# Optimization experiments

Hardware: AMD Instinct MI355X
Metric: run time of the kernel (lower is better)

## Reference

```python
import jax, jax.numpy as jnp
from jax import lax
import numpy as np

DEPTH = 6
DIM = 512            # embed_dim
DI = 768             # d_inner = int(1.5 * 512)
B = 64
IMG = 224
P = 16               # patch size == stride
HW = 14              # patches per side
NP = HW * HW         # 196


def _ln(x, w, b, eps=1e-5):
    m = jnp.mean(x, axis=-1, keepdims=True)
    v = jnp.var(x, axis=-1, keepdims=True)
    return (x - m) / jnp.sqrt(v + eps) * w + b


def _mamba(x, in_w, out_w, cw, cb, dw, db, A, D):
    # x: (N, L, DIM); in_w: (2*DI, DIM); out_w: (DIM, DI); cw: (DI, 3)
    xz = jnp.einsum('nlc,dc->nld', x, in_w)          # (N, L, 2*DI)
    xi, z = jnp.split(xz, 2, axis=-1)
    # depthwise conv1d, kernel=3, padding=1
    xp = jnp.pad(xi, ((0, 0), (1, 1), (0, 0)))
    xc = xp[:, :-2] * cw[:, 0] + xp[:, 1:-1] * cw[:, 1] + xp[:, 2:] * cw[:, 2] + cb
    xc = jax.nn.silu(xc)
    dt = jax.nn.softplus(jnp.einsum('nld,ed->nle', xc, dw) + db)
    Ae = jnp.exp(A * dt)                              # A < 0, dt > 0 -> stable
    y = jnp.cumsum(xc * dt * Ae, axis=1) * Ae + xc * D
    y = y * jax.nn.silu(z)
    return jnp.einsum('nld,cd->nlc', y, out_w)


def _forward(x, patch_w, patch_b, cls_token, pos_embed,
             blk_norm_w, blk_norm_b,
             mh_in_w, mh_out_w, mh_conv_w, mh_conv_b, mh_dt_w, mh_dt_b, mh_A, mh_D,
             mv_in_w, mv_out_w, mv_conv_w, mv_conv_b, mv_dt_w, mv_dt_b, mv_A, mv_D,
             fus_w, fus_b, ss_norm_w, ss_norm_b, fn_w, fn_b):
    Bsz = x.shape[0]
    # patch embed: Conv2d(3, DIM, k=16, s=16)
    feat = lax.conv_general_dilated(x, patch_w, window_strides=(P, P), padding='VALID',
                                    dimension_numbers=('NCHW', 'OIHW', 'NCHW'))
    feat = feat + patch_b[None, :, None, None]
    feat = feat.reshape(Bsz, DIM, NP).transpose(0, 2, 1)  # (B, 196, DIM)
    tok = jnp.concatenate([jnp.broadcast_to(cls_token, (Bsz, 1, DIM)), feat], axis=1)
    tok = tok + pos_embed                                  # (B, 197, DIM)
    for i in range(DEPTH):
        cls = tok[:, :1]
        pt = tok[:, 1:]
        pn = _ln(pt, blk_norm_w[i], blk_norm_b[i])
        p2 = pn.reshape(Bsz, HW, HW, DIM)
        # horizontal scan: rows as sequences
        yh = _mamba(p2.reshape(Bsz * HW, HW, DIM),
                    mh_in_w[i], mh_out_w[i], mh_conv_w[i], mh_conv_b[i],
                    mh_dt_w[i], mh_dt_b[i], mh_A[i], mh_D[i]).reshape(Bsz, HW, HW, DIM)
        # vertical scan: columns as sequences
        xv = p2.transpose(0, 2, 1, 3).reshape(Bsz * HW, HW, DIM)
        yv = _mamba(xv,
                    mv_in_w[i], mv_out_w[i], mv_conv_w[i], mv_conv_b[i],
                    mv_dt_w[i], mv_dt_b[i], mv_A[i], mv_D[i])
        yv = yv.reshape(Bsz, HW, HW, DIM).transpose(0, 2, 1, 3)
        yc = jnp.concatenate([yh, yv], axis=-1)            # (B, H, W, 2*DIM)
        yf = jnp.einsum('bhwk,ck->bhwc', yc, fus_w[i]) + fus_b[i]
        p_out = _ln(yf + p2, ss_norm_w[i], ss_norm_b[i]).reshape(Bsz, NP, DIM)
        cls_out = cls + _ln(cls, blk_norm_w[i], blk_norm_b[i])
        tok = jnp.concatenate([cls_out, p_out], axis=1)
    return _ln(tok, fn_w, fn_b)


def setup_inputs() -> dict:
    key = jax.random.key(0)
    ks = jax.random.split(key, 32)
    s = 0.02
    d = {}
    d['x'] = jax.random.normal(ks[0], (B, 3, IMG, IMG), jnp.float32)
    d['patch_w'] = jax.random.normal(ks[1], (DIM, 3, P, P), jnp.float32) * s
    d['patch_b'] = jnp.zeros((DIM,), jnp.float32)
    d['cls_token'] = jax.random.normal(ks[2], (1, 1, DIM), jnp.float32) * s
    d['pos_embed'] = jax.random.normal(ks[3], (1, NP + 1, DIM), jnp.float32) * s
    d['blk_norm_w'] = jnp.ones((DEPTH, DIM), jnp.float32)
    d['blk_norm_b'] = jnp.zeros((DEPTH, DIM), jnp.float32)
    for pfx, base in (('mh', 4), ('mv', 12)):
        d[pfx + '_in_w'] = jax.random.normal(ks[base + 0], (DEPTH, 2 * DI, DIM), jnp.float32) * s
        d[pfx + '_out_w'] = jax.random.normal(ks[base + 1], (DEPTH, DIM, DI), jnp.float32) * s
        d[pfx + '_conv_w'] = jax.random.normal(ks[base + 2], (DEPTH, DI, 3), jnp.float32) * 0.2
        d[pfx + '_conv_b'] = jnp.zeros((DEPTH, DI), jnp.float32)
        d[pfx + '_dt_w'] = jax.random.normal(ks[base + 3], (DEPTH, DI, DI), jnp.float32) * s
        d[pfx + '_dt_b'] = jnp.zeros((DEPTH, DI), jnp.float32)
        d[pfx + '_A'] = -jax.random.uniform(ks[base + 4], (DEPTH, DI), jnp.float32) * 0.1
        d[pfx + '_D'] = jnp.ones((DEPTH, DI), jnp.float32)
    d['fus_w'] = jax.random.normal(ks[20], (DEPTH, DIM, 2 * DIM), jnp.float32) * s
    d['fus_b'] = jnp.zeros((DEPTH, DIM), jnp.float32)
    d['ss_norm_w'] = jnp.ones((DEPTH, DIM), jnp.float32)
    d['ss_norm_b'] = jnp.zeros((DEPTH, DIM), jnp.float32)
    d['fn_w'] = jnp.ones((DIM,), jnp.float32)
    d['fn_b'] = jnp.zeros((DIM,), jnp.float32)
    return d


def reference(x, patch_w, patch_b, cls_token, pos_embed,
              blk_norm_w, blk_norm_b,
              mh_in_w, mh_out_w, mh_conv_w, mh_conv_b, mh_dt_w, mh_dt_b, mh_A, mh_D,
              mv_in_w, mv_out_w, mv_conv_w, mv_conv_b, mv_dt_w, mv_dt_b, mv_A, mv_D,
              fus_w, fus_b, ss_norm_w, ss_norm_b, fn_w, fn_b):
    return _forward(x, patch_w, patch_b, cls_token, pos_embed,
                    blk_norm_w, blk_norm_b,
                    mh_in_w, mh_out_w, mh_conv_w, mh_conv_b, mh_dt_w, mh_dt_b, mh_A, mh_D,
                    mv_in_w, mv_out_w, mv_conv_w, mv_conv_b, mv_dt_w, mv_dt_b, mv_A, mv_D,
                    fus_w, fus_b, ss_norm_w, ss_norm_b, fn_w, fn_b)
```

## Files before the change

kernel.cpp:

```cpp
#include <hip/hip_runtime.h>
#include <cstdint>


using u16 = unsigned short;
typedef __attribute__((ext_vector_type(8))) short   bfrag;
typedef __attribute__((ext_vector_type(4))) float   ffrag;
typedef __attribute__((ext_vector_type(8))) u16     u16x8;
typedef __attribute__((ext_vector_type(4))) u16     u16x4;

__device__ __forceinline__ float b2f(u16 u) {
  union { float f; uint32_t i; } c; c.i = ((uint32_t)u) << 16; return c.f;
}
__device__ __forceinline__ u16 f2b(float f) {
  union { float f; uint32_t i; } c; c.f = f;
  uint32_t r = c.i + 0x7FFFu + ((c.i >> 16) & 1u);
  return (u16)(r >> 16);
}

#define LOG2E 1.44269504f
#define LN2   0.69314718f
__device__ __forceinline__ float fexp(float x) {
  return __builtin_amdgcn_exp2f(x * LOG2E);
}
__device__ __forceinline__ float fsigmoid(float x) {
  return __builtin_amdgcn_rcpf(1.f + __builtin_amdgcn_exp2f(-x * LOG2E));
}
__device__ __forceinline__ float fsilu(float x) { return x * fsigmoid(x); }
__device__ __forceinline__ float fsoftplus(float x) {
  float e = __builtin_amdgcn_exp2f(-fabsf(x) * LOG2E);
  return fmaxf(x, 0.f) + LN2 * __builtin_amdgcn_logf(1.f + e);
}

__device__ __forceinline__ void gl_lds16(const u16* g, u16* l) {
  __builtin_amdgcn_global_load_lds(
      (const __attribute__((address_space(1))) void*)g,
      (__attribute__((address_space(3))) void*)l,
      16, 0, 0);
}

__global__ __launch_bounds__(256, 2)
void gemm_dual(const u16* __restrict__ A, const u16* __restrict__ W1,
               const u16* __restrict__ W2, u16* __restrict__ C,
               int K, int lda, int ldc, int nsplit, int acol2, int ccol2)
{
  __shared__ u16 As[2][128 * 64];
  __shared__ u16 Bs[2][128 * 64];

  const int total = gridDim.x * gridDim.y;
  const int flat  = blockIdx.y * gridDim.x + blockIdx.x;
  const int chunk = total >> 3;
  const int f2    = (flat & 7) * chunk + (flat >> 3);
  const int bx    = f2 % gridDim.x;
  const int by    = f2 / gridDim.x;

  const bool second = bx >= nsplit;
  const u16* W     = second ? W2 : W1;
  const int n0l    = (bx - (second ? nsplit : 0)) * 128;
  const int acol   = second ? acol2 : 0;
  const int ccol0  = n0l + (second ? ccol2 : 0);
  const int m0     = by * 128;

  const int tid  = threadIdx.x;
  const int lane = tid & 63;
  const int wv   = tid >> 6;
  const int wm   = wv >> 1;
  const int wn   = wv & 1;

  const int lr   = lane >> 3;
  const int lc   = lane & 7;
  const int kcol = (lc ^ lr) << 3;

  const size_t abase = (size_t)(m0 + wv * 32 + lr) * lda + acol + kcol;
  const size_t wbase = (size_t)(n0l + wv * 32 + lr) * K + kcol;

  const ffrag fz = {0.f, 0.f, 0.f, 0.f};
  ffrag acc[4][4];
#pragma unroll
  for (int i = 0; i < 4; ++i)
#pragma unroll
    for (int j = 0; j < 4; ++j) acc[i][j] = fz;

  const int fr = lane & 15;
  const int fq = lane >> 4;

  auto stage = [&](int kb, int buf) {
#pragma unroll
    for (int i = 0; i < 4; ++i)
      gl_lds16(A + abase + (size_t)(i * 8) * lda + kb, &As[buf][(wv * 4 + i) * 512]);
#pragma unroll
    for (int i = 0; i < 4; ++i)
      gl_lds16(W + wbase + (size_t)(i * 8) * K + kb, &Bs[buf][(wv * 4 + i) * 512]);
  };

  const int nk = K >> 6;
  stage(0, 0);
  __syncthreads();

  for (int t = 0; t < nk; ++t) {
    const int cur = t & 1;
    if (t + 1 < nk) stage((t + 1) * 64, cur ^ 1);

#pragma unroll
    for (int ks = 0; ks < 2; ++ks) {
      bfrag af[4], bfr[4];
#pragma unroll
      for (int t4 = 0; t4 < 4; ++t4) {
        int r  = wm * 64 + t4 * 16 + fr;
        int ca = ((ks * 4 + fq) ^ (r & 7)) << 3;
        af[t4]  = *(const bfrag*)&As[cur][r * 64 + ca];
        int n  = wn * 64 + t4 * 16 + fr;
        int cb = ((ks * 4 + fq) ^ (n & 7)) << 3;
        bfr[t4] = *(const bfrag*)&Bs[cur][n * 64 + cb];
      }
#pragma unroll
      for (int i = 0; i < 4; ++i)
#pragma unroll
        for (int j = 0; j < 4; ++j)
          acc[i][j] = __builtin_amdgcn_mfma_f32_16x16x32_bf16(
              af[i], bfr[j], acc[i][j], 0, 0, 0);
    }
    __syncthreads();
  }

#pragma unroll
  for (int i = 0; i < 4; ++i)
#pragma unroll
    for (int j = 0; j < 4; ++j)
#pragma unroll
      for (int rg = 0; rg < 4; ++rg) {
        int row = m0 + wm * 64 + i * 16 + fq * 4 + rg;
        int col = ccol0 + wn * 64 + j * 16 + fr;
        C[(size_t)row * ldc + col] = f2b(acc[i][j][rg]);
      }
}

__global__ __launch_bounds__(256, 2)
void gemm_wprep(const u16* __restrict__ WB, const u16* __restrict__ OT,
                u16* __restrict__ WF)
{
  __shared__ u16 As[128 * 64];
  __shared__ u16 Bs[128 * 64];

  const int z = blockIdx.z, L = z >> 1, path = z & 1;
  const u16* A = WB + (size_t)L * 4063232 + 3538944;
  const u16* W = OT + (size_t)z * 393216;
  u16* C = WF + (size_t)L * 786432;

  const int m0 = blockIdx.y * 128, n0l = blockIdx.x * 128;
  const int acol = path * 512, ccol = path * 768;

  const int tid  = threadIdx.x;
  const int lane = tid & 63;
  const int wv   = tid >> 6;
  const int wm   = wv >> 1;
  const int wn   = wv & 1;
  const int lr   = lane >> 3;
  const int lc   = lane & 7;
  const int kcol = (lc ^ lr) << 3;

  const size_t abase = (size_t)(m0 + wv * 32 + lr) * 1024 + acol + kcol;
  const size_t wbase = (size_t)(n0l + wv * 32 + lr) * 512 + kcol;

  const ffrag fz = {0.f, 0.f, 0.f, 0.f};
  ffrag acc[4][4];
#pragma unroll
  for (int i = 0; i < 4; ++i)
#pragma unroll
    for (int j = 0; j < 4; ++j) acc[i][j] = fz;

  const int fr = lane & 15;
  const int fq = lane >> 4;

  for (int kb = 0; kb < 512; kb += 64) {
#pragma unroll
    for (int i = 0; i < 4; ++i)
      gl_lds16(A + abase + (size_t)(i * 8) * 1024 + kb, &As[(wv * 4 + i) * 512]);
#pragma unroll
    for (int i = 0; i < 4; ++i)
      gl_lds16(W + wbase + (size_t)(i * 8) * 512 + kb, &Bs[(wv * 4 + i) * 512]);
    __syncthreads();

#pragma unroll
    for (int ks = 0; ks < 2; ++ks) {
      bfrag af[4], bfr[4];
#pragma unroll
      for (int t = 0; t < 4; ++t) {
        int r  = wm * 64 + t * 16 + fr;
        int ca = ((ks * 4 + fq) ^ (r & 7)) << 3;
        af[t]  = *(const bfrag*)&As[r * 64 + ca];
        int n  = wn * 64 + t * 16 + fr;
        int cb = ((ks * 4 + fq) ^ (n & 7)) << 3;
        bfr[t] = *(const bfrag*)&Bs[n * 64 + cb];
      }
#pragma unroll
      for (int i = 0; i < 4; ++i)
#pragma unroll
        for (int j = 0; j < 4; ++j)
          acc[i][j] = __builtin_amdgcn_mfma_f32_16x16x32_bf16(
              af[i], bfr[j], acc[i][j], 0, 0, 0);
    }
    __syncthreads();
  }

#pragma unroll
  for (int i = 0; i < 4; ++i)
#pragma unroll
    for (int j = 0; j < 4; ++j)
#pragma unroll
      for (int rg = 0; rg < 4; ++rg) {
        int row = m0 + wm * 64 + i * 16 + fq * 4 + rg;
        int col = ccol + n0l + wn * 64 + j * 16 + fr;
        C[(size_t)row * 1536 + col] = f2b(acc[i][j][rg]);
      }
}

__global__ __launch_bounds__(256)
void k_transp(const float* __restrict__ mho, const float* __restrict__ mvo,
              u16* __restrict__ OT)
{
  __shared__ float ld[32][33];
  const int z = blockIdx.z, L = z >> 1, path = z & 1;
  const float* src = (path ? mvo : mho) + (size_t)L * 393216;
  u16* dst = OT + (size_t)z * 393216;
  const int tx = threadIdx.x & 31, ty = threadIdx.x >> 5;
  const int dx = blockIdx.x * 32, cy = blockIdx.y * 32;
#pragma unroll
  for (int i = 0; i < 4; ++i)
    ld[ty + 8 * i][tx] = src[(size_t)(cy + ty + 8 * i) * 768 + dx + tx];
  __syncthreads();
#pragma unroll
  for (int i = 0; i < 4; ++i)
    dst[(size_t)(dx + ty + 8 * i) * 512 + cy + tx] = f2b(ld[tx][ty + 8 * i]);
}

__global__ __launch_bounds__(256)
void k_cvt_all(const float* __restrict__ mhi, const float* __restrict__ mhd,
               const float* __restrict__ mvi, const float* __restrict__ mvd,
               const float* __restrict__ fus, u16* __restrict__ dst)
{
  size_t e = ((size_t)blockIdx.x * 256 + threadIdx.x) * 8;
  int L = (int)(e / 3276800);
  int r = (int)(e - (size_t)L * 3276800);
  const float* s; int off; int dsto;
  if      (r <  786432) { s = mhi + (size_t)L * 786432; off = r;           dsto = r; }
  else if (r < 1376256) { s = mhd + (size_t)L * 589824; off = r -  786432; dsto = r; }
  else if (r < 2162688) { s = mvi + (size_t)L * 786432; off = r - 1376256; dsto = r + 393216; }
  else if (r < 2752512) { s = mvd + (size_t)L * 589824; off = r - 2162688; dsto = r + 393216; }
  else                  { s = fus + (size_t)L * 524288; off = r - 2752512; dsto = r + 786432; }
  float4 a = *(const float4*)(s + off);
  float4 b = *(const float4*)(s + off + 4);
  u16x8 o;
  o[0] = f2b(a.x); o[1] = f2b(a.y); o[2] = f2b(a.z); o[3] = f2b(a.w);
  o[4] = f2b(b.x); o[5] = f2b(b.y); o[6] = f2b(b.z); o[7] = f2b(b.w);
  *(u16x8*)(dst + (size_t)L * 4063232 + dsto) = o;
}

__global__ __launch_bounds__(256)
void k_cvt1(const float* __restrict__ s, u16* __restrict__ dst)
{
  int e = (blockIdx.x * 256 + threadIdx.x) * 8;
  float4 a = *(const float4*)(s + e);
  float4 b = *(const float4*)(s + e + 4);
  u16x8 o;
  o[0] = f2b(a.x); o[1] = f2b(a.y); o[2] = f2b(a.z); o[3] = f2b(a.w);
  o[4] = f2b(b.x); o[5] = f2b(b.y); o[6] = f2b(b.z); o[7] = f2b(b.w);
  *(u16x8*)(dst + e) = o;
}

__global__ __launch_bounds__(256) void k_im2col(const float* __restrict__ x,
                                                u16* __restrict__ im)
{
  int idx = blockIdx.x * 256 + threadIdx.x;
  int r = idx % 96, p = idx / 96;
  int b = p / 196, q = p - b * 196;
  int ph = q / 14, pw = q - ph * 14;
  int k = r * 8;
  int c = k >> 8, k2 = k & 255;
  int i = k2 >> 4, j = k2 & 15;
  const float* src = x + (((size_t)(b * 3 + c) * 224 + ph * 16 + i) * 224
                          + pw * 16 + j);
  float4 a = *(const float4*)src;
  float4 d = *(const float4*)(src + 4);
  u16x8 o;
  o[0] = f2b(a.x); o[1] = f2b(a.y); o[2] = f2b(a.z); o[3] = f2b(a.w);
  o[4] = f2b(d.x); o[5] = f2b(d.y); o[6] = f2b(d.z); o[7] = f2b(d.w);
  *(u16x8*)(im + (size_t)p * 768 + k) = o;
}

__global__ __launch_bounds__(256)
void k_addbias_ln(u16* __restrict__ TOK, const float* __restrict__ pb,
                  const float* __restrict__ pos, const float* __restrict__ w,
                  const float* __restrict__ b)
{
  int row  = blockIdx.x * 4 + (threadIdx.x >> 6);
  int lane = threadIdx.x & 63;
  int base = lane * 8;
  int tpos = 1 + (row % 196);
  u16* p = TOK + (size_t)row * 512 + base;
  u16x8 t = *(u16x8*)p;
  const float* pv = pos + (size_t)tpos * 512 + base;
  float v[8]; float s = 0.f, qq = 0.f;
#pragma unroll
  for (int i = 0; i < 8; ++i) {
    v[i] = b2f(t[i]) + pb[base + i] + pv[i];
    s += v[i]; qq += v[i] * v[i];
  }
#pragma unroll
  for (int o = 32; o; o >>= 1) { s += __shfl_xor(s, o, 64); qq += __shfl_xor(qq, o, 64); }
  float mean = s * (1.f / 512.f);
  float rstd = rsqrtf(qq * (1.f / 512.f) - mean * mean + 1e-5f);
  u16x8 ov;
#pragma unroll
  for (int i = 0; i < 8; ++i)
    ov[i] = f2b((v[i] - mean) * rstd * w[base + i] + b[base + i]);
  *(u16x8*)p = ov;
}

__global__ __launch_bounds__(256) void k_ln_fuse(const u16* __restrict__ YF,
                                                 u16* __restrict__ TOK,
                                                 const float* __restrict__ fb,
                                                 const float* __restrict__ w,
                                                 const float* __restrict__ b)
{
  int row  = blockIdx.x * 4 + (threadIdx.x >> 6);
  int lane = threadIdx.x & 63;
  int base = lane * 8;
  const u16* yf = YF + (size_t)row * 512 + base;
  u16* tp = TOK + (size_t)row * 512 + base;
  u16x8 yv = *(const u16x8*)yf;
  u16x8 tv = *(u16x8*)tp;
  float v[8]; float s = 0.f, qq = 0.f;
#pragma unroll
  for (int i = 0; i < 8; ++i) {
    v[i] = b2f(yv[i]) + fb[base + i] + b2f(tv[i]);
    s += v[i]; qq += v[i] * v[i];
  }
#pragma unroll
  for (int o = 32; o; o >>= 1) { s += __shfl_xor(s, o, 64); qq += __shfl_xor(qq, o, 64); }
  float mean = s * (1.f / 512.f);
  float rstd = rsqrtf(qq * (1.f / 512.f) - mean * mean + 1e-5f);
  u16x8 ov;
#pragma unroll
  for (int i = 0; i < 8; ++i)
    ov[i] = f2b((v[i] - mean) * rstd * w[base + i] + b[base + i]);
  *(u16x8*)tp = ov;
}

__global__ __launch_bounds__(256)
void k_ln_fuse2(const u16* __restrict__ YF, u16* __restrict__ TOK,
                const float* __restrict__ fb, const float* __restrict__ w1,
                const float* __restrict__ b1, const float* __restrict__ w2,
                const float* __restrict__ b2)
{
  int row  = blockIdx.x * 4 + (threadIdx.x >> 6);
  int lane = threadIdx.x & 63;
  int base = lane * 8;
  const u16* yf = YF + (size_t)row * 512 + base;
  u16* tp = TOK + (size_t)row * 512 + base;
  u16x8 yv = *(const u16x8*)yf;
  u16x8 tv = *(u16x8*)tp;
  float v[8]; float s = 0.f, qq = 0.f;
#pragma unroll
  for (int i = 0; i < 8; ++i) {
    v[i] = b2f(yv[i]) + fb[base + i] + b2f(tv[i]);
    s += v[i]; qq += v[i] * v[i];
  }
#pragma unroll
  for (int o = 32; o; o >>= 1) { s += __shfl_xor(s, o, 64); qq += __shfl_xor(qq, o, 64); }
  float mean = s * (1.f / 512.f);
  float rstd = rsqrtf(qq * (1.f / 512.f) - mean * mean + 1e-5f);
  float s2 = 0.f, q2 = 0.f;
#pragma unroll
  for (int i = 0; i < 8; ++i) {
    v[i] = (v[i] - mean) * rstd * w1[base + i] + b1[base + i];
    s2 += v[i]; q2 += v[i] * v[i];
  }
#pragma unroll
  for (int o = 32; o; o >>= 1) { s2 += __shfl_xor(s2, o, 64); q2 += __shfl_xor(q2, o, 64); }
  float m2 = s2 * (1.f / 512.f);
  float r2 = rsqrtf(q2 * (1.f / 512.f) - m2 * m2 + 1e-5f);
  u16x8 ov;
#pragma unroll
  for (int i = 0; i < 8; ++i)
    ov[i] = f2b((v[i] - m2) * r2 * w2[base + i] + b2[base + i]);
  *(u16x8*)tp = ov;
}

__global__ __launch_bounds__(256)
void k_conv_hv(const u16* __restrict__ XZ,
               const float* __restrict__ cwh, const float* __restrict__ cbh,
               const float* __restrict__ cwv, const float* __restrict__ cbv,
               u16* __restrict__ XC)
{
  int idx = blockIdx.x * 256 + threadIdx.x;
  int half = idx >= 86016;
  int t = idx - (half ? 86016 : 0);
  int dp = t % 96, sq = t / 96;
  int d0 = dp * 8;
  int rowbase, rowstride;
  if (!half) { rowbase = sq * 14; rowstride = 1; }
  else       { int b = sq / 14, wq = sq - b * 14; rowbase = b * 196 + wq; rowstride = 14; }
  const float* cw = half ? cwv : cwh;
  const float* cb = half ? cbv : cbh;
  int xio = half ? 1536 : 0, xco = half ? 768 : 0;
  float w0[8], w1[8], w2[8], bc[8];
#pragma unroll
  for (int i = 0; i < 8; ++i) {
    w0[i] = cw[(d0 + i) * 3 + 0];
    w1[i] = cw[(d0 + i) * 3 + 1];
    w2[i] = cw[(d0 + i) * 3 + 2];
    bc[i] = cb[d0 + i];
  }
  u16x8 cu = *(const u16x8*)&XZ[(size_t)rowbase * 3072 + xio + d0];
  float p[8], c[8], n[8];
#pragma unroll
  for (int i = 0; i < 8; ++i) { p[i] = 0.f; c[i] = b2f(cu[i]); }
#pragma unroll
  for (int l = 0; l < 14; ++l) {
    int row = rowbase + l * rowstride;
    if (l < 13) {
      u16x8 nu = *(const u16x8*)&XZ[(size_t)(row + rowstride) * 3072 + xio + d0];
#pragma unroll
      for (int i = 0; i < 8; ++i) n[i] = b2f(nu[i]);
    } else {
#pragma unroll
      for (int i = 0; i < 8; ++i) n[i] = 0.f;
    }
    u16x8 ov;
#pragma unroll
    for (int i = 0; i < 8; ++i)
      ov[i] = f2b(fsilu(p[i] * w0[i] + c[i] * w1[i] + n[i] * w2[i] + bc[i]));
    *(u16x8*)&XC[(size_t)row * 1536 + xco + d0] = ov;
#pragma unroll
    for (int i = 0; i < 8; ++i) { p[i] = c[i]; c[i] = n[i]; }
  }
}

__global__ __launch_bounds__(256)
void k_scan_hv(const u16* __restrict__ XZ, u16* __restrict__ XC,
               const float* __restrict__ dtbh, const float* __restrict__ Ah,
               const float* __restrict__ Dh,
               const float* __restrict__ dtbv, const float* __restrict__ Av,
               const float* __restrict__ Dv)
{
  int idx = blockIdx.x * 256 + threadIdx.x;
  int half = idx >= 86016;
  int t = idx - (half ? 86016 : 0);
  int dp = t % 96, sq = t / 96;
  int d0 = dp * 8;
  int rowbase, rowstride;
  if (!half) { rowbase = sq * 14; rowstride = 1; }
  else       { int b = sq / 14, wq = sq - b * 14; rowbase = b * 196 + wq; rowstride = 14; }
  int xio = half ? 1536 : 0, xco = half ? 768 : 0;
  const float* dtb = half ? dtbv : dtbh;
  const float* Ap  = half ? Av : Ah;
  const float* Dp  = half ? Dv : Dh;
  float db[8], Aa[8], Da[8], r[8];
#pragma unroll
  for (int i = 0; i < 8; ++i) {
    db[i] = dtb[d0 + i]; Aa[i] = Ap[d0 + i]; Da[i] = Dp[d0 + i]; r[i] = 0.f;
  }
#pragma unroll
  for (int l = 0; l < 14; ++l) {
    int row = rowbase + l * rowstride;
    size_t zb  = (size_t)row * 3072 + xio;
    size_t cbo = (size_t)row * 1536 + xco;
    u16x8 xcu = *(const u16x8*)&XC[cbo + d0];
    u16x8 dtu = *(const u16x8*)&XZ[zb + d0];
    u16x8 zu  = *(const u16x8*)&XZ[zb + 768 + d0];
    u16x8 ov;
#pragma unroll
    for (int i = 0; i < 8; ++i) {
      float xc = b2f(xcu[i]);
      float dt = fsoftplus(b2f(dtu[i]) + db[i]);
      float ae = fexp(Aa[i] * dt);
      r[i] += xc * dt * ae;
      float z = b2f(zu[i]);
      float y = (r[i] * ae + xc * Da[i]) * (z * fsigmoid(z));
      ov[i] = f2b(y);
    }
    *(u16x8*)&XC[cbo + d0] = ov;
  }
}

__global__ void k_cls(const float* __restrict__ cls_tok,
                      const float* __restrict__ pos,
                      const float* __restrict__ bw, const float* __restrict__ bb,
                      float* __restrict__ CLS)
{
  __shared__ float rs[8], rq[8], stat[2];
  int n = threadIdx.x;
  float v = cls_tok[n] + pos[n];
  for (int l = 0; l < 6; ++l) {
    float s = v, q = v * v;
#pragma unroll
    for (int o = 32; o; o >>= 1) { s += __shfl_xor(s, o, 64); q += __shfl_xor(q, o, 64); }
    if ((n & 63) == 0) { rs[n >> 6] = s; rq[n >> 6] = q; }
    __syncthreads();
    if (n == 0) {
      float S = 0.f, Q = 0.f;
      for (int i = 0; i < 8; ++i) { S += rs[i]; Q += rq[i]; }
      float m = S * (1.f / 512.f);
      stat[0] = m; stat[1] = rsqrtf(Q * (1.f / 512.f) - m * m + 1e-5f);
    }
    __syncthreads();
    float u = (v - stat[0]) * stat[1] * bw[l * 512 + n] + bb[l * 512 + n];
    v = v + u;
    __syncthreads();
  }
  CLS[n] = v;
}

__global__ __launch_bounds__(256) void k_final(const u16* __restrict__ TOK,
                                               const float* __restrict__ CLS,
                                               const float* __restrict__ w,
                                               const float* __restrict__ b,
                                               float* __restrict__ out)
{
  int row  = blockIdx.x * 4 + (threadIdx.x >> 6);
  int lane = threadIdx.x & 63;
  int bi = row / 197;
  int t  = row - bi * 197;
  int base = lane * 8;
  float v[8]; float s = 0.f, qq = 0.f;
  if (t == 0) {
#pragma unroll
    for (int i = 0; i < 8; ++i) v[i] = CLS[base + i];
  } else {
    const u16* src = TOK + ((size_t)bi * 196 + (t - 1)) * 512 + base;
    u16x8 tv = *(const u16x8*)src;
#pragma unroll
    for (int i = 0; i < 8; ++i) v[i] = b2f(tv[i]);
  }
#pragma unroll
  for (int i = 0; i < 8; ++i) { s += v[i]; qq += v[i] * v[i]; }
#pragma unroll
  for (int o = 32; o; o >>= 1) { s += __shfl_xor(s, o, 64); qq += __shfl_xor(qq, o, 64); }
  float mean = s * (1.f / 512.f);
  float rstd = rsqrtf(qq * (1.f / 512.f) - mean * mean + 1e-5f);
  float* op = out + (size_t)row * 512 + base;
#pragma unroll
  for (int i = 0; i < 8; ++i)
    op[i] = (v[i] - mean) * rstd * w[base + i] + b[base + i];
}

extern "C" void kernel_launch(void* const* d_in, const int* in_sizes, int n_in,
                              void* d_out, int out_size, void* d_ws, size_t ws_size,
                              hipStream_t stream)
{
  const float* x        = (const float*)d_in[0];
  const float* patch_w  = (const float*)d_in[1];
  const float* patch_b  = (const float*)d_in[2];
  const float* cls_tok  = (const float*)d_in[3];
  const float* pos      = (const float*)d_in[4];
  const float* blk_w    = (const float*)d_in[5];
  const float* blk_b    = (const float*)d_in[6];
  const float* mh_in_w  = (const float*)d_in[7];
  const float* mh_out_w = (const float*)d_in[8];
  const float* mh_cw    = (const float*)d_in[9];
  const float* mh_cb    = (const float*)d_in[10];
  const float* mh_dtw   = (const float*)d_in[11];
  const float* mh_dtb   = (const float*)d_in[12];
  const float* mh_A     = (const float*)d_in[13];
  const float* mh_D     = (const float*)d_in[14];
  const float* mv_in_w  = (const float*)d_in[15];
  const float* mv_out_w = (const float*)d_in[16];
  const float* mv_cw    = (const float*)d_in[17];
  const float* mv_cb    = (const float*)d_in[18];
  const float* mv_dtw   = (const float*)d_in[19];
  const float* mv_dtb   = (const float*)d_in[20];
  const float* mv_A     = (const float*)d_in[21];
  const float* mv_D     = (const float*)d_in[22];
  const float* fus_w    = (const float*)d_in[23];
  const float* fus_b    = (const float*)d_in[24];
  const float* ss_w     = (const float*)d_in[25];
  const float* ss_b     = (const float*)d_in[26];
  const float* fn_w     = (const float*)d_in[27];
  const float* fn_b     = (const float*)d_in[28];

  char* ws = (char*)d_ws;
  u16*   TOK  = (u16*)  (ws);
  u16*   XZHV = (u16*)  (ws +  12845056);
  u16*   XCHV = (u16*)  (ws +  89915392);
  u16*   WB   = (u16*)  (ws + 128450560);
  u16*   WP   = (u16*)  (ws + 177209344);
  u16*   OT   = (u16*)  (ws + 178782208);
  u16*   WF   = (u16*)  (ws + 188219392);
  float* CLS  = (float*)(ws + 197656576);
  u16*   IM   = XCHV;
  u16*   YF   = XZHV;

  const size_t LS = 4063232;
  const size_t oMHI = 0, oMHD = 786432, oMVI = 1769472, oMVD = 2555904;

  k_cvt_all<<<9600, 256, 0, stream>>>(mh_in_w, mh_dtw,
                                      mv_in_w, mv_dtw, fus_w, WB);
  k_transp<<<dim3(24, 16, 12), 256, 0, stream>>>(mh_out_w, mv_out_w, OT);
  gemm_wprep<<<dim3(6, 4, 12), 256, 0, stream>>>(WB, OT, WF);
  k_cvt1<<<192, 256, 0, stream>>>(patch_w, WP);
  k_im2col<<<4704, 256, 0, stream>>>(x, IM);
  gemm_dual<<<dim3(4, 98), 256, 0, stream>>>(IM, WP, WP, TOK,
                                             768, 768, 512, 4, 0, 0);
  k_addbias_ln<<<3136, 256, 0, stream>>>(TOK, patch_b, pos, blk_w, blk_b);
  k_cls<<<1, 512, 0, stream>>>(cls_tok, pos, blk_w, blk_b, CLS);

  for (int L = 0; L < 6; ++L) {
    const u16* wl = WB + (size_t)L * LS;

    gemm_dual<<<dim3(24, 98), 256, 0, stream>>>(
        TOK, wl + oMHI, wl + oMVI, XZHV, 512, 512, 3072, 12, 0, 1536);
    k_conv_hv<<<672, 256, 0, stream>>>(XZHV, mh_cw + L * 2304, mh_cb + L * 768,
                                       mv_cw + L * 2304, mv_cb + L * 768, XCHV);
    gemm_dual<<<dim3(12, 98), 256, 0, stream>>>(
        XCHV, wl + oMHD, wl + oMVD, XZHV, 768, 1536, 3072, 6, 768, 1536);
    k_scan_hv<<<672, 256, 0, stream>>>(XZHV, XCHV,
                                       mh_dtb + L * 768, mh_A + L * 768, mh_D + L * 768,
                                       mv_dtb + L * 768, mv_A + L * 768, mv_D + L * 768);
    gemm_dual<<<dim3(4, 98), 256, 0, stream>>>(
        XCHV, WF + (size_t)L * 786432, WF + (size_t)L * 786432, YF,
        1536, 1536, 512, 4, 0, 0);
    if (L < 5) {
      k_ln_fuse2<<<3136, 256, 0, stream>>>(YF, TOK, fus_b + L * 512,
                                           ss_w + L * 512, ss_b + L * 512,
                                           blk_w + (L + 1) * 512, blk_b + (L + 1) * 512);
    } else {
      k_ln_fuse<<<3136, 256, 0, stream>>>(YF, TOK, fus_b + L * 512,
                                          ss_w + L * 512, ss_b + L * 512);
    }
  }

  k_final<<<3152, 256, 0, stream>>>(TOK, CLS, fn_w, fn_b, (float*)d_out);
  (void)in_sizes; (void)n_in; (void)out_size; (void)ws_size;
}
```

Measured before the change: 1.311 ms.

## Drop GEMM double buffering and add 64x128-tile kernel for N=512 GEMMs

Removes the LDS double-buffer prefetch from gemm_dual, so each K step now loads, syncs, computes and syncs again. It also adds gemm_n512, which uses 64x128 tiles to double the block count (4x196) for the N=512 GEMMs (patch embed and output projection), giving better CU occupancy on those small-N launches. The cost is that global-to-LDS loads no longer overlap MFMA compute in either kernel, which could slow the large in-projection GEMMs.

```diff
diff --git a/kernel.cpp b/kernel.cpp
--- a/kernel.cpp
+++ b/kernel.cpp
@@ -6,7 +6,6 @@
 typedef __attribute__((ext_vector_type(8))) short   bfrag;
 typedef __attribute__((ext_vector_type(4))) float   ffrag;
 typedef __attribute__((ext_vector_type(8))) u16     u16x8;
-typedef __attribute__((ext_vector_type(4))) u16     u16x4;
 
 __device__ __forceinline__ float b2f(u16 u) {
   union { float f; uint32_t i; } c; c.i = ((uint32_t)u) << 16; return c.f;
@@ -43,8 +42,8 @@
                const u16* __restrict__ W2, u16* __restrict__ C,
                int K, int lda, int ldc, int nsplit, int acol2, int ccol2)
 {
-  __shared__ u16 As[2][128 * 64];
-  __shared__ u16 Bs[2][128 * 64];
+  __shared__ u16 As[128 * 64];
+  __shared__ u16 Bs[128 * 64];
 
   const int total = gridDim.x * gridDim.y;
   const int flat  = blockIdx.y * gridDim.x + blockIdx.x;
@@ -83,34 +82,26 @@
   const int fr = lane & 15;
   const int fq = lane >> 4;
 
-  auto stage = [&](int kb, int buf) {
+  for (int kb = 0; kb < K; kb += 64) {
 #pragma unroll
     for (int i = 0; i < 4; ++i)
-      gl_lds16(A + abase + (size_t)(i * 8) * lda + kb, &As[buf][(wv * 4 + i) * 512]);
+      gl_lds16(A + abase + (size_t)(i * 8) * lda + kb, &As[(wv * 4 + i) * 512]);
 #pragma unroll
     for (int i = 0; i < 4; ++i)
-      gl_lds16(W + wbase + (size_t)(i * 8) * K + kb, &Bs[buf][(wv * 4 + i) * 512]);
-  };
-
-  const int nk = K >> 6;
-  stage(0, 0);
-  __syncthreads();
-
-  for (int t = 0; t < nk; ++t) {
-    const int cur = t & 1;
-    if (t + 1 < nk) stage((t + 1) * 64, cur ^ 1);
+      gl_lds16(W + wbase + (size_t)(i * 8) * K + kb, &Bs[(wv * 4 + i) * 512]);
+    __syncthreads();
 
 #pragma unroll
     for (int ks = 0; ks < 2; ++ks) {
       bfrag af[4], bfr[4];
 #pragma unroll
-      for (int t4 = 0; t4 < 4; ++t4) {
-        int r  = wm * 64 + t4 * 16 + fr;
+      for (int t = 0; t < 4; ++t) {
+        int r  = wm * 64 + t * 16 + fr;
         int ca = ((ks * 4 + fq) ^ (r & 7)) << 3;
-        af[t4]  = *(const bfrag*)&As[cur][r * 64 + ca];
-        int n  = wn * 64 + t4 * 16 + fr;
+        af[t]  = *(const bfrag*)&As[r * 64 + ca];
+        int n  = wn * 64 + t * 16 + fr;
         int cb = ((ks * 4 + fq) ^ (n & 7)) << 3;
-        bfr[t4] = *(const bfrag*)&Bs[cur][n * 64 + cb];
+        bfr[t] = *(const bfrag*)&Bs[n * 64 + cb];
       }
 #pragma unroll
       for (int i = 0; i < 4; ++i)
@@ -130,6 +121,92 @@
       for (int rg = 0; rg < 4; ++rg) {
         int row = m0 + wm * 64 + i * 16 + fq * 4 + rg;
         int col = ccol0 + wn * 64 + j * 16 + fr;
+        C[(size_t)row * ldc + col] = f2b(acc[i][j][rg]);
+      }
+}
+
+__global__ __launch_bounds__(256, 2)
+void gemm_n512(const u16* __restrict__ A, const u16* __restrict__ W,
+               u16* __restrict__ C, int K, int lda, int ldc)
+{
+  __shared__ u16 As[64 * 64];
+  __shared__ u16 Bs[128 * 64];
+
+  const int total = gridDim.x * gridDim.y;
+  const int flat  = blockIdx.y * gridDim.x + blockIdx.x;
+  const int chunk = total >> 3;
+  const int f2    = (flat & 7) * chunk + (flat >> 3);
+  const int bx    = f2 % gridDim.x;
+  const int by    = f2 / gridDim.x;
+
+  const int n0l = bx * 128;
+  const int m0  = by * 64;
+
+  const int tid  = threadIdx.x;
+  const int lane = tid & 63;
+  const int wv   = tid >> 6;
+  const int wm   = wv >> 1;
+  const int wn   = wv & 1;
+
+  const int lr   = lane >> 3;
+  const int lc   = lane & 7;
+  const int kcol = (lc ^ lr) << 3;
+
+  const size_t abase = (size_t)(m0 + wv * 16 + lr) * lda + kcol;
+  const size_t wbase = (size_t)(n0l + wv * 32 + lr) * K + kcol;
+
+  const ffrag fz = {0.f, 0.f, 0.f, 0.f};
+  ffrag acc[2][4];
+#pragma unroll
+  for (int i = 0; i < 2; ++i)
+#pragma unroll
+    for (int j = 0; j < 4; ++j) acc[i][j] = fz;
+
+  const int fr = lane & 15;
+  const int fq = lane >> 4;
+
+  for (int kb = 0; kb < K; kb += 64) {
+#pragma unroll
+    for (int i = 0; i < 2; ++i)
+      gl_lds16(A + abase + (size_t)(i * 8) * lda + kb, &As[(wv * 2 + i) * 512]);
+#pragma unroll
+    for (int i = 0; i < 4; ++i)
+      gl_lds16(W + wbase + (size_t)(i * 8) * K + kb, &Bs[(wv * 4 + i) * 512]);
+    __syncthreads();
+
+#pragma unroll
+    for (int ks = 0; ks < 2; ++ks) {
+      bfrag af[2], bfr[4];
+#pragma unroll
+      for (int t = 0; t < 2; ++t) {
+        int r  = wm * 32 + t * 16 + fr;
+        int ca = ((ks * 4 + fq) ^ (r & 7)) << 3;
+        af[t]  = *(const bfrag*)&As[r * 64 + ca];
+      }
+#pragma unroll
+      for (int t = 0; t < 4; ++t) {
+        int n  = wn * 64 + t * 16 + fr;
+        int cb = ((ks * 4 + fq) ^ (n & 7)) << 3;
+        bfr[t] = *(const bfrag*)&Bs[n * 64 + cb];
+      }
+#pragma unroll
+      for (int i = 0; i < 2; ++i)
+#pragma unroll
+        for (int j = 0; j < 4; ++j)
+          acc[i][j] = __builtin_amdgcn_mfma_f32_16x16x32_bf16(
+              af[i], bfr[j], acc[i][j], 0, 0, 0);
+    }
+    __syncthreads();
+  }
+
+#pragma unroll
+  for (int i = 0; i < 2; ++i)
+#pragma unroll
+    for (int j = 0; j < 4; ++j)
+#pragma unroll
+      for (int rg = 0; rg < 4; ++rg) {
+        int row = m0 + wm * 32 + i * 16 + fq * 4 + rg;
+        int col = n0l + wn * 64 + j * 16 + fr;
         C[(size_t)row * ldc + col] = f2b(acc[i][j][rg]);
       }
 }
@@ -599,8 +676,7 @@
   gemm_wprep<<<dim3(6, 4, 12), 256, 0, stream>>>(WB, OT, WF);
   k_cvt1<<<192, 256, 0, stream>>>(patch_w, WP);
   k_im2col<<<4704, 256, 0, stream>>>(x, IM);
-  gemm_dual<<<dim3(4, 98), 256, 0, stream>>>(IM, WP, WP, TOK,
-                                             768, 768, 512, 4, 0, 0);
+  gemm_n512<<<dim3(4, 196), 256, 0, stream>>>(IM, WP, TOK, 768, 768, 512);
   k_addbias_ln<<<3136, 256, 0, stream>>>(TOK, patch_b, pos, blk_w, blk_b);
   k_cls<<<1, 512, 0, stream>>>(cls_tok, pos, blk_w, blk_b, CLS);
 
@@ -616,9 +692,8 @@
     k_scan_hv<<<672, 256, 0, stream>>>(XZHV, XCHV,
                                        mh_dtb + L * 768, mh_A + L * 768, mh_D + L * 768,
                                        mv_dtb + L * 768, mv_A + L * 768, mv_D + L * 768);
-    gemm_dual<<<dim3(4, 98), 256, 0, stream>>>(
-        XCHV, WF + (size_t)L * 786432, WF + (size_t)L * 786432, YF,
-        1536, 1536, 512, 4, 0, 0);
+    gemm_n512<<<dim3(4, 196), 256, 0, stream>>>(
+        XCHV, WF + (size_t)L * 786432, YF, 1536, 1536, 512);
     if (L < 5) {
       k_ln_fuse2<<<3136, 256, 0, stream>>>(YF, TOK, fus_b + L * 512,
                                            ss_w + L * 512, ss_b + L * 512,
```

Measured after the change: 1.293 ms. About the same (-1.4%).
